# Kernel tuning notes

Hardware: AMD Instinct MI355X
Metric: run time of the kernel (lower is better)

The kernel has to match this reference:

```python
import jax, jax.numpy as jnp
import numpy as np
from jax import lax

MAX_OBJ = 100
IOU_THRES = 0.45
SCORE_THRES = 0.25
MAX_WH = 7680.0

# xywh -> xyxy conversion matrix (same as ONNX_ORT.convert_matrix)
CONVERT = jnp.array([[1, 0, 1, 0],
                     [0, 1, 0, 1],
                     [-0.5, 0, 0.5, 0],
                     [0, -0.5, 0, 0.5]], dtype=jnp.float32)


def _iou_one_vs_all(box, boxes):
    # box: [4] xyxy, boxes: [N,4] xyxy
    x1 = jnp.maximum(box[0], boxes[:, 0])
    y1 = jnp.maximum(box[1], boxes[:, 1])
    x2 = jnp.minimum(box[2], boxes[:, 2])
    y2 = jnp.minimum(box[3], boxes[:, 3])
    inter = jnp.clip(x2 - x1, 0.0) * jnp.clip(y2 - y1, 0.0)
    a = (box[2] - box[0]) * (box[3] - box[1])
    b = (boxes[:, 2] - boxes[:, 0]) * (boxes[:, 3] - boxes[:, 1])
    return inter / (a + b - inter + 1e-9)


def _nms_indices(nmsbox, max_score):
    # Greedy class-offset NMS; returns [MAX_OBJ] indices, -1 for padding.
    valid0 = max_score >= SCORE_THRES

    def step(valid, _):
        s = jnp.where(valid, max_score, -1.0)
        i = jnp.argmax(s)
        ok = s[i] >= SCORE_THRES
        iou = _iou_one_vs_all(nmsbox[i], nmsbox)
        valid = valid & (iou <= IOU_THRES)
        valid = valid.at[i].set(False)
        return valid, jnp.where(ok, i, -1)

    _, idxs = lax.scan(step, valid0, None, length=MAX_OBJ)
    return idxs


def _forward(x1, x2, num_labels1, num_labels2):
    B, N1, _ = x1.shape
    N2 = x2.shape[1]
    # pad x1 class scores with zeros for model2's labels (appended at end)
    x1p = jnp.concatenate([x1, jnp.zeros((B, N1, num_labels2), x1.dtype)], axis=2)
    # pad x2: insert zeros for model1's labels between conf and its own classes
    x2p = jnp.concatenate([x2[:, :, 0:5],
                           jnp.zeros((B, N2, num_labels1), x2.dtype),
                           x2[:, :, 5:]], axis=2)
    x = jnp.concatenate([x1p, x2p], axis=1)  # [B, N1+N2, 5+C1+C2]

    boxes = x[:, :, :4] @ CONVERT            # xywh -> xyxy, [B,N,4]
    conf = x[:, :, 4:5]
    scores = x[:, :, 5:] * conf              # [B,N,C]
    max_score = scores.max(axis=2)           # [B,N]
    cat_id = scores.argmax(axis=2)           # [B,N]
    # class-offset boxes so NMS is class-aware
    nmsbox = boxes + cat_id[..., None].astype(boxes.dtype) * MAX_WH

    idxs = jax.vmap(_nms_indices)(lax.stop_gradient(nmsbox),
                                  lax.stop_gradient(max_score))  # [B,MAX_OBJ]
    mask = idxs >= 0
    si = jnp.maximum(idxs, 0)
    sel_boxes = jnp.take_along_axis(boxes, si[..., None], axis=1)      # [B,MAX_OBJ,4]
    sel_cat = jnp.take_along_axis(cat_id, si, axis=1).astype(boxes.dtype)
    sel_score = jnp.take_along_axis(max_score, si, axis=1)

    mf = mask.astype(boxes.dtype)
    Xcol = jnp.where(mask, jnp.arange(B)[:, None], -1).astype(boxes.dtype)
    out = jnp.concatenate([Xcol[..., None],
                           sel_boxes * mf[..., None],
                           (sel_cat * mf)[..., None],
                           (sel_score * mf)[..., None]], axis=2)
    return out.reshape(B * MAX_OBJ, 7)


def setup_inputs() -> dict:
    key = jax.random.key(0)
    k1, k2 = jax.random.split(key)
    x1 = jax.random.uniform(k1, (4, 25200, 85), dtype=jnp.float32)
    x2 = jax.random.uniform(k2, (4, 25200, 25), dtype=jnp.float32)
    return {"x1": x1, "x2": x2, "num_labels1": 80, "num_labels2": 20}


def reference(x1, x2, num_labels1, num_labels2):
    return _forward(x1, x2, num_labels1, num_labels2)
```

## Files before the change

### kernel.cpp

```cpp
#include <hip/hip_runtime.h>
#include <stdint.h>

#pragma clang fp contract(off)

#define BATCH 4
#define N1 25200
#define NROW 50400
#define NCLS 100
#define TOT (BATCH*NROW)
#define CAPB 2048
#define SCORE_T 0.25f
#define IOU_T 0.45f
#define MAXWH 7680.0f

#define X1_SLAB 64
#define X1_SPB 394
#define X2_SLAB 256
#define X2_SPB 99

#define NKK 12600
#define NIT 49
#define NTAIL 56

typedef unsigned long long u64;

__device__ __forceinline__ u64 pack_key(unsigned sb, int n, int cid) {
    return ((u64)sb << 32) | ((u64)(unsigned)((n ^ 0xFFFF) & 0xFFFF) << 8) | (u64)(unsigned)cid;
}

__device__ __forceinline__ bool sup_test(float inter, float sum) {
    float d = (sum - inter) + 1e-9f;
    float t1 = IOU_T * d;
    bool hi = inter > t1 * 1.00001f;
    bool lo = inter < t1 * 0.99999f;
    if (__builtin_expect(!(hi || lo), 0)) return (inter / d) > IOU_T;
    return hi;
}

__device__ __forceinline__ float rl(float v, int srcLane) {
    return __int_as_float(__builtin_amdgcn_readlane(__float_as_int(v), srcLane));
}

__device__ __forceinline__ void blk2bucket(int blk, int& b, int& c) {
    if (blk < BATCH * 20) { b = blk / 20; c = 80 + (blk - b * 20); }
    else { int z = blk - BATCH * 20; b = z / 80; c = z - b * 80; }
}

__device__ __forceinline__ int prefix_ge(const u64* list, int cnt, u64 T) {
    int lo = 0, hi = cnt;
    while (lo < hi) {
        int mid = (lo + hi) >> 1;
        if (list[mid] >= T) lo = mid + 1; else hi = mid;
    }
    return lo;
}

__device__ __forceinline__ void sort_desc(u64* sk, int L, int t) {
    bool act = (t * 8) < L;
    u64 r[8];
    if (act) {
#pragma unroll
        for (int e = 0; e < 8; ++e) r[e] = sk[t * 8 + e];
    }
    for (int k = 2; k <= L; k <<= 1) {
        for (int j = k >> 1; j > 0; j >>= 1) {
            if (j >= 512) {
                if (act) {
#pragma unroll
                    for (int e = 0; e < 8; ++e) sk[t * 8 + e] = r[e];
                }
                __syncthreads();
                if (act) {
                    bool iAmLo = (t & (j >> 3)) == 0;
                    bool descSeg = (t & (k >> 3)) == 0;
                    bool takeMax = (descSeg == iAmLo);
#pragma unroll
                    for (int e = 0; e < 8; ++e) {
                        u64 u = r[e];
                        u64 v = sk[(t * 8 + e) ^ j];
                        bool uGE = (u >= v);
                        r[e] = (takeMax == uGE) ? u : v;
                    }
                }
                __syncthreads();
            } else if (j >= 8) {
                if (act) {
                    int dt = j >> 3;
                    bool iAmLo = (t & dt) == 0;
                    bool descSeg = (t & (k >> 3)) == 0;
                    bool takeMax = (descSeg == iAmLo);
#pragma unroll
                    for (int e = 0; e < 8; ++e) {
                        u64 u = r[e];
                        u64 v = __shfl_xor(u, dt, 64);
                        bool uGE = (u >= v);
                        r[e] = (takeMax == uGE) ? u : v;
                    }
                }
            } else {
                if (act) {
#pragma unroll
                    for (int e = 0; e < 8; ++e) {
                        if (!(e & j)) {
                            int e2 = e | j;
                            bool descSeg = (k >= 8) ? ((t & (k >> 3)) == 0)
                                                    : ((e & k) == 0);
                            u64 lo = r[e], hi = r[e2];
                            bool sw = descSeg ? (lo < hi) : (lo > hi);
                            if (sw) { r[e] = hi; r[e2] = lo; }
                        }
                    }
                }
            }
        }
    }
    if (act) {
#pragma unroll
        for (int e = 0; e < 8; ++e) sk[t * 8 + e] = r[e];
    }
    __syncthreads();
}

__global__ __launch_bounds__(256) void k_rows(const float* __restrict__ x1,
                                              const float* __restrict__ x2,
                                              float4* __restrict__ boxes4,
                                              u64* __restrict__ rowKey) {
    __shared__ float4 ld4[1600];
    float* ld = (float*)ld4;
    int blk = blockIdx.x;
    int t = threadIdx.x;
    const int NX1 = BATCH * X1_SPB;
    if (blk < NX1) {
        int b = blk / X1_SPB, s = blk - b * X1_SPB;
        int r0 = s * X1_SLAB;
        int nr = min(X1_SLAB, N1 - r0);
        const float4* src = (const float4*)(x1 + ((size_t)b * N1 + r0) * 85);
        int count4 = (nr * 85) >> 2;
        for (int i = t; i < count4; i += 256) ld4[i] = src[i];
        __syncthreads();
        int row = t >> 2, sub = t & 3;
        if (row < nr) {
            const float* p = ld + row * 85;
            float conf = p[4];
            u64 key = 0ULL;
            int base = sub * 20;
            for (int c = 0; c < 20; ++c) {
                int j = base + c;
                float v = p[5 + j] * conf;
                u64 kk = ((u64)__float_as_uint(v) << 32) | (unsigned)~(unsigned)j;
                if (kk > key) key = kk;
            }
            u64 o;
            o = __shfl_xor(key, 1, 64); if (o > key) key = o;
            o = __shfl_xor(key, 2, 64); if (o > key) key = o;
            if (sub == 0) {
                float best = __uint_as_float((unsigned)(key >> 32));
                int bestj = ~(unsigned)key;
                int n = r0 + row;
                int r = b * NROW + n;
                u64 outk = 0ULL;
                if (best >= SCORE_T) {
                    float cx = p[0], cy = p[1], w = p[2], h = p[3];
                    boxes4[r] = make_float4(cx - 0.5f * w, cy - 0.5f * h,
                                            cx + 0.5f * w, cy + 0.5f * h);
                    outk = pack_key((unsigned)(key >> 32), n, bestj);
                }
                rowKey[r] = outk;
            }
        }
    } else {
        int blk2 = blk - NX1;
        int b = blk2 / X2_SPB, s = blk2 - b * X2_SPB;
        int r0 = s * X2_SLAB;
        int nr = min(X2_SLAB, N1 - r0);
        const float4* src = (const float4*)(x2 + ((size_t)b * N1 + r0) * 25);
        int count4 = (nr * 25) >> 2;
        for (int i = t; i < count4; i += 256) ld4[i] = src[i];
        __syncthreads();
        if (t < nr) {
            const float* p = ld + t * 25;
            float conf = p[4];
            float best = 0.0f; int bestj = 0;
            for (int j2 = 0; j2 < 20; ++j2) {
                float v = p[5 + j2] * conf;
                if (v > best) { best = v; bestj = 80 + j2; }
            }
            int n = N1 + r0 + t;
            int r = b * NROW + n;
            u64 outk = 0ULL;
            if (best >= SCORE_T) {
                float cx = p[0], cy = p[1], w = p[2], h = p[3];
                boxes4[r] = make_float4(cx - 0.5f * w, cy - 0.5f * h,
                                        cx + 0.5f * w, cy + 0.5f * h);
                outk = pack_key(__float_as_uint(best), n, bestj);
            }
            rowKey[r] = outk;
        }
    }
}

__global__ __launch_bounds__(256) void k_nms(const float4* __restrict__ boxes4,
                                             const u64* __restrict__ rowKey,
                                             u64* __restrict__ accKey,
                                             int* __restrict__ accCnt) {
    __shared__ u64 sk[CAPB];
    __shared__ float4 cQ[CAPB];
    __shared__ float4 accQ[100];
    __shared__ float accA[100];
    __shared__ int wsum[4];
    int b, c; blk2bucket(blockIdx.x, b, c);
    int bucket = b * NCLS + c;
    int t = threadIdx.x;
    int lane = t & 63, wid = t >> 6;

    int rowBase = (c >= 80) ? N1 : 0;
    const ulonglong2* rk2 = (const ulonglong2*)(rowKey + (size_t)b * NROW + rowBase);

    int cnt = 0;
#pragma unroll 4
    for (int it = 0; it < NIT; ++it) {
        ulonglong2 kk = rk2[t + (it << 8)];
        cnt += ((kk.x != 0ULL) && ((int)(kk.x & 0xFF) == c)) ? 1 : 0;
        cnt += ((kk.y != 0ULL) && ((int)(kk.y & 0xFF) == c)) ? 1 : 0;
    }
    if (t < NTAIL) {
        ulonglong2 kk = rk2[NIT * 256 + t];
        cnt += ((kk.x != 0ULL) && ((int)(kk.x & 0xFF) == c)) ? 1 : 0;
        cnt += ((kk.y != 0ULL) && ((int)(kk.y & 0xFF) == c)) ? 1 : 0;
    }
    int inc = cnt;
    for (int o = 1; o < 64; o <<= 1) {
        int v = __shfl_up(inc, o, 64);
        if (lane >= o) inc += v;
    }
    if (lane == 63) wsum[wid] = inc;
    __syncthreads();
    int cnt0 = wsum[0] + wsum[1] + wsum[2] + wsum[3];
    if (cnt0 == 0) { if (t == 0) accCnt[bucket] = 0; return; }
    int woff = 0;
    for (int w = 0; w < wid; ++w) woff += wsum[w];
    int pos = woff + inc - cnt;
    cnt0 = min(cnt0, CAPB);
#pragma unroll 4
    for (int it = 0; it < NIT; ++it) {
        ulonglong2 kk = rk2[t + (it << 8)];
        if ((kk.x != 0ULL) && ((int)(kk.x & 0xFF) == c)) { if (pos < CAPB) sk[pos] = kk.x; ++pos; }
        if ((kk.y != 0ULL) && ((int)(kk.y & 0xFF) == c)) { if (pos < CAPB) sk[pos] = kk.y; ++pos; }
    }
    if (t < NTAIL) {
        ulonglong2 kk = rk2[NIT * 256 + t];
        if ((kk.x != 0ULL) && ((int)(kk.x & 0xFF) == c)) { if (pos < CAPB) sk[pos] = kk.x; ++pos; }
        if ((kk.y != 0ULL) && ((int)(kk.y & 0xFF) == c)) { if (pos < CAPB) sk[pos] = kk.y; ++pos; }
    }
    int L = 512; while (L < cnt0) L <<= 1;
    for (int i = cnt0 + t; i < L; i += 256) sk[i] = 0ULL;
    __syncthreads();
    sort_desc(sk, L, t);

    float off = (float)c * MAXWH;
    for (int i = t; i < cnt0; i += 256) {
        u64 k = sk[i];
        int n = 0xFFFF ^ (int)((k >> 8) & 0xFFFF);
        float4 v = boxes4[b * NROW + n];
        v.x += off; v.y += off; v.z += off; v.w += off;
        cQ[i] = v;
    }
    __syncthreads();
    if (t >= 64) return;

    int m = 0;
    for (int base = 0; base < cnt0 && m < 100; base += 64) {
        int j = base + lane;
        bool alive = (j < cnt0);
        float4 a = make_float4(0.f, 0.f, 0.f, 0.f);
        float aA = 0.f; u64 myKey = 0ULL;
        if (alive) {
            myKey = sk[j];
            a = cQ[j];
            aA = (a.z - a.x) * (a.w - a.y);
        }
        int k2 = 0;
        while (k2 < m) {
            if (__ballot(alive) == 0ULL) break;
            int rem = m - k2;
            if (rem >= 8) {
#pragma unroll
                for (int u = 0; u < 8; ++u) {
                    float4 q = accQ[k2 + u];
                    float qa = accA[k2 + u];
                    float xx1 = fmaxf(a.x, q.x), yy1 = fmaxf(a.y, q.y);
                    float xx2 = fminf(a.z, q.z), yy2 = fminf(a.w, q.w);
                    float inter = fmaxf(xx2 - xx1, 0.f) * fmaxf(yy2 - yy1, 0.f);
                    alive = alive && !sup_test(inter, qa + aA);
                }
                k2 += 8;
            } else {
                for (int u = 0; u < rem; ++u) {
                    float4 q = accQ[k2 + u];
                    float qa = accA[k2 + u];
                    float xx1 = fmaxf(a.x, q.x), yy1 = fmaxf(a.y, q.y);
                    float xx2 = fminf(a.z, q.z), yy2 = fminf(a.w, q.w);
                    float inter = fmaxf(xx2 - xx1, 0.f) * fmaxf(yy2 - yy1, 0.f);
                    alive = alive && !sup_test(inter, qa + aA);
                }
                k2 = m;
            }
        }
        u64 av = __ballot(alive);
        while (av != 0ULL && m < 100) {
            int f = __builtin_ctzll(av);
            float qx = rl(a.x, f), qy = rl(a.y, f);
            float qz = rl(a.z, f), qw = rl(a.w, f);
            float qa = rl(aA, f);
            if (lane == f) {
                accQ[m] = a; accA[m] = aA;
                accKey[(size_t)bucket * 100 + m] = myKey;
                alive = false;
            }
            ++m;
            if (alive) {
                float xx1 = fmaxf(a.x, qx), yy1 = fmaxf(a.y, qy);
                float xx2 = fminf(a.z, qz), yy2 = fminf(a.w, qw);
                float inter = fmaxf(xx2 - xx1, 0.f) * fmaxf(yy2 - yy1, 0.f);
                alive = !sup_test(inter, qa + aA);
            }
            av = __ballot(alive);
        }
    }
    if (lane == 0) accCnt[bucket] = m;
}

__global__ __launch_bounds__(256) void k_merge(const float4* __restrict__ boxes4,
                                               const u64* __restrict__ accKey,
                                               const int* __restrict__ accCnt,
                                               float* __restrict__ out) {
    __shared__ u64 sk[1024];
    __shared__ u64 head[NCLS];
    __shared__ int cnts[NCLS];
    __shared__ int pc[NCLS];
    int b = blockIdx.x, t = threadIdx.x;
    const u64* base = accKey + (size_t)b * NCLS * 100;
    if (t < NCLS) {
        int cc = accCnt[b * NCLS + t];
        cnts[t] = cc;
        head[t] = (cc > 0) ? base[t * 100] : 0ULL;
    }
    __syncthreads();
    int S = 0, ne = 0; u64 mn = ~0ULL;
    for (int c = 0; c < NCLS; ++c) {
        int cc = cnts[c];
        S += cc;
        if (cc > 0) { ++ne; u64 h = head[c]; if (h < mn) mn = h; }
    }
    u64 T;
    bool bisect;
    if (S <= 900)            { T = 0ULL; bisect = false; }
    else if (ne == NCLS)     { T = mn;   bisect = false; }
    else                     { T = 0ULL; bisect = true;  }
    if (t < NCLS) pc[t] = bisect ? 0 : prefix_ge(base + t * 100, cnts[t], T);
    __syncthreads();
    int G = 0;
    for (int c = 0; c < NCLS; ++c) G += pc[c];
    if (G > 1000) bisect = true;
    if (bisect) {
        u64 lo = 0ULL, hi = ~0ULL;
        for (int it = 0; it < 64; ++it) {
            u64 mid = lo + ((hi - lo) >> 1);
            if (t < NCLS) pc[t] = prefix_ge(base + t * 100, cnts[t], mid);
            __syncthreads();
            int cnt = 0;
            for (int c = 0; c < NCLS; ++c) cnt += pc[c];
            if (cnt >= 100 && cnt <= 1000) { T = mid; G = cnt; break; }
            if (cnt < 100) hi = mid; else lo = mid;
            __syncthreads();
        }
    }
    if (t < NCLS) {
        int off = 0;
        for (int c = 0; c < t; ++c) off += pc[c];
        int p = pc[t];
        for (int j = 0; j < p; ++j) sk[off + j] = base[t * 100 + j];
    }
    for (int i = G + t; i < 1024; i += 256) sk[i] = 0ULL;
    __syncthreads();
    sort_desc(sk, 1024, t);
    if (t < 100) {
        u64 k = sk[t];
        float* o7 = out + (size_t)(b * 100 + t) * 7;
        if (k == 0ULL) {
            o7[0] = -1.0f;
            o7[1] = 0.0f; o7[2] = 0.0f; o7[3] = 0.0f;
            o7[4] = 0.0f; o7[5] = 0.0f; o7[6] = 0.0f;
        } else {
            int n = 0xFFFF ^ (int)((k >> 8) & 0xFFFF);
            int cid = (int)(k & 0xFF);
            float4 bx = boxes4[b * NROW + n];
            o7[0] = (float)b;
            o7[1] = bx.x; o7[2] = bx.y; o7[3] = bx.z; o7[4] = bx.w;
            o7[5] = (float)cid;
            o7[6] = __uint_as_float((unsigned)(k >> 32));
        }
    }
}

extern "C" void kernel_launch(void* const* d_in, const int* in_sizes, int n_in,
                              void* d_out, int out_size, void* d_ws, size_t ws_size,
                              hipStream_t stream) {
    const float* x1 = (const float*)d_in[0];
    const float* x2 = (const float*)d_in[1];
    float* out = (float*)d_out;

    float4* boxes4 = (float4*)d_ws;
    u64* rowKey = (u64*)(boxes4 + TOT);
    u64* accKey = rowKey + TOT;
    int* accCnt = (int*)(accKey + (size_t)BATCH * NCLS * 100);

    int rowBlocks = BATCH * X1_SPB + BATCH * X2_SPB;
    k_rows<<<rowBlocks, 256, 0, stream>>>(x1, x2, boxes4, rowKey);
    k_nms<<<BATCH * NCLS, 256, 0, stream>>>(boxes4, rowKey, accKey, accCnt);
    k_merge<<<BATCH, 256, 0, stream>>>(boxes4, accKey, accCnt, out);
}
```

Baseline: 148.3 us.

## Bucket candidate keys per class with atomics instead of rescanning all rows

The row kernel now appends each passing candidate's key to a per-(batch,class) bucket using an atomic fill counter. This replaces the dense rowKey array that every NMS block had to scan twice (count, then compact). Each NMS block then reads only its own bucket, and the per-candidate shared-memory writes are deferred until after the greedy loop. This adds atomic contention, a memset launch and a lower per-class capacity (CAPB 1280). Bucket order is now nondeterministic, but the sort restores it. The selected box's area is also recomputed rather than read across lanes.

```diff
diff --git a/kernel.cpp b/kernel.cpp
--- a/kernel.cpp
+++ b/kernel.cpp
@@ -8,7 +8,7 @@
 #define NROW 50400
 #define NCLS 100
 #define TOT (BATCH*NROW)
-#define CAPB 2048
+#define CAPB 1280
 #define SCORE_T 0.25f
 #define IOU_T 0.45f
 #define MAXWH 7680.0f
@@ -17,10 +17,6 @@
 #define X1_SPB 394
 #define X2_SLAB 256
 #define X2_SPB 99
-
-#define NKK 12600
-#define NIT 49
-#define NTAIL 56
 
 typedef unsigned long long u64;
 
@@ -124,7 +120,8 @@
 __global__ __launch_bounds__(256) void k_rows(const float* __restrict__ x1,
                                               const float* __restrict__ x2,
                                               float4* __restrict__ boxes4,
-                                              u64* __restrict__ rowKey) {
+                                              u64* __restrict__ csrKey,
+                                              int* __restrict__ fill) {
     __shared__ float4 ld4[1600];
     float* ld = (float*)ld4;
     int blk = blockIdx.x;
@@ -156,16 +153,18 @@
             if (sub == 0) {
                 float best = __uint_as_float((unsigned)(key >> 32));
                 int bestj = ~(unsigned)key;
-                int n = r0 + row;
-                int r = b * NROW + n;
-                u64 outk = 0ULL;
                 if (best >= SCORE_T) {
+                    int n = r0 + row;
+                    int r = b * NROW + n;
                     float cx = p[0], cy = p[1], w = p[2], h = p[3];
                     boxes4[r] = make_float4(cx - 0.5f * w, cy - 0.5f * h,
                                             cx + 0.5f * w, cy + 0.5f * h);
-                    outk = pack_key((unsigned)(key >> 32), n, bestj);
-                }
-                rowKey[r] = outk;
+                    int bucket = b * NCLS + bestj;
+                    int pos = atomicAdd(&fill[bucket], 1);
+                    if (pos < CAPB)
+                        csrKey[(size_t)bucket * CAPB + pos] =
+                            pack_key((unsigned)(key >> 32), n, bestj);
+                }
             }
         }
     } else {
@@ -185,78 +184,42 @@
                 float v = p[5 + j2] * conf;
                 if (v > best) { best = v; bestj = 80 + j2; }
             }
-            int n = N1 + r0 + t;
-            int r = b * NROW + n;
-            u64 outk = 0ULL;
             if (best >= SCORE_T) {
+                int n = N1 + r0 + t;
+                int r = b * NROW + n;
                 float cx = p[0], cy = p[1], w = p[2], h = p[3];
                 boxes4[r] = make_float4(cx - 0.5f * w, cy - 0.5f * h,
                                         cx + 0.5f * w, cy + 0.5f * h);
-                outk = pack_key(__float_as_uint(best), n, bestj);
-            }
-            rowKey[r] = outk;
+                int bucket = b * NCLS + bestj;
+                int pos = atomicAdd(&fill[bucket], 1);
+                if (pos < CAPB)
+                    csrKey[(size_t)bucket * CAPB + pos] =
+                        pack_key(__float_as_uint(best), n, bestj);
+            }
         }
     }
 }
 
 __global__ __launch_bounds__(256) void k_nms(const float4* __restrict__ boxes4,
-                                             const u64* __restrict__ rowKey,
+                                             const u64* __restrict__ csrKey,
+                                             const int* __restrict__ fill,
                                              u64* __restrict__ accKey,
                                              int* __restrict__ accCnt) {
-    __shared__ u64 sk[CAPB];
+    __shared__ u64 sk[2048];
     __shared__ float4 cQ[CAPB];
     __shared__ float4 accQ[100];
     __shared__ float accA[100];
-    __shared__ int wsum[4];
     int b, c; blk2bucket(blockIdx.x, b, c);
     int bucket = b * NCLS + c;
     int t = threadIdx.x;
-    int lane = t & 63, wid = t >> 6;
-
-    int rowBase = (c >= 80) ? N1 : 0;
-    const ulonglong2* rk2 = (const ulonglong2*)(rowKey + (size_t)b * NROW + rowBase);
-
-    int cnt = 0;
-#pragma unroll 4
-    for (int it = 0; it < NIT; ++it) {
-        ulonglong2 kk = rk2[t + (it << 8)];
-        cnt += ((kk.x != 0ULL) && ((int)(kk.x & 0xFF) == c)) ? 1 : 0;
-        cnt += ((kk.y != 0ULL) && ((int)(kk.y & 0xFF) == c)) ? 1 : 0;
-    }
-    if (t < NTAIL) {
-        ulonglong2 kk = rk2[NIT * 256 + t];
-        cnt += ((kk.x != 0ULL) && ((int)(kk.x & 0xFF) == c)) ? 1 : 0;
-        cnt += ((kk.y != 0ULL) && ((int)(kk.y & 0xFF) == c)) ? 1 : 0;
-    }
-    int inc = cnt;
-    for (int o = 1; o < 64; o <<= 1) {
-        int v = __shfl_up(inc, o, 64);
-        if (lane >= o) inc += v;
-    }
-    if (lane == 63) wsum[wid] = inc;
-    __syncthreads();
-    int cnt0 = wsum[0] + wsum[1] + wsum[2] + wsum[3];
+    int lane = t & 63;
+    int cnt0 = min(fill[bucket], CAPB);
     if (cnt0 == 0) { if (t == 0) accCnt[bucket] = 0; return; }
-    int woff = 0;
-    for (int w = 0; w < wid; ++w) woff += wsum[w];
-    int pos = woff + inc - cnt;
-    cnt0 = min(cnt0, CAPB);
-#pragma unroll 4
-    for (int it = 0; it < NIT; ++it) {
-        ulonglong2 kk = rk2[t + (it << 8)];
-        if ((kk.x != 0ULL) && ((int)(kk.x & 0xFF) == c)) { if (pos < CAPB) sk[pos] = kk.x; ++pos; }
-        if ((kk.y != 0ULL) && ((int)(kk.y & 0xFF) == c)) { if (pos < CAPB) sk[pos] = kk.y; ++pos; }
-    }
-    if (t < NTAIL) {
-        ulonglong2 kk = rk2[NIT * 256 + t];
-        if ((kk.x != 0ULL) && ((int)(kk.x & 0xFF) == c)) { if (pos < CAPB) sk[pos] = kk.x; ++pos; }
-        if ((kk.y != 0ULL) && ((int)(kk.y & 0xFF) == c)) { if (pos < CAPB) sk[pos] = kk.y; ++pos; }
-    }
+    const u64* src = csrKey + (size_t)bucket * CAPB;
     int L = 512; while (L < cnt0) L <<= 1;
-    for (int i = cnt0 + t; i < L; i += 256) sk[i] = 0ULL;
+    for (int i = t; i < L; i += 256) sk[i] = (i < cnt0) ? src[i] : 0ULL;
     __syncthreads();
     sort_desc(sk, L, t);
-
     float off = (float)c * MAXWH;
     for (int i = t; i < cnt0; i += 256) {
         u64 k = sk[i];
@@ -307,24 +270,25 @@
             }
         }
         u64 av = __ballot(alive);
+        int accIdx = -1;
         while (av != 0ULL && m < 100) {
             int f = __builtin_ctzll(av);
             float qx = rl(a.x, f), qy = rl(a.y, f);
             float qz = rl(a.z, f), qw = rl(a.w, f);
-            float qa = rl(aA, f);
-            if (lane == f) {
-                accQ[m] = a; accA[m] = aA;
-                accKey[(size_t)bucket * 100 + m] = myKey;
-                alive = false;
-            }
+            if (lane == f) { accIdx = m; alive = false; }
             ++m;
             if (alive) {
+                float qa = (qz - qx) * (qw - qy);
                 float xx1 = fmaxf(a.x, qx), yy1 = fmaxf(a.y, qy);
                 float xx2 = fminf(a.z, qz), yy2 = fminf(a.w, qw);
                 float inter = fmaxf(xx2 - xx1, 0.f) * fmaxf(yy2 - yy1, 0.f);
                 alive = !sup_test(inter, qa + aA);
             }
             av = __ballot(alive);
+        }
+        if (accIdx >= 0) {
+            accQ[accIdx] = a; accA[accIdx] = aA;
+            accKey[(size_t)bucket * 100 + accIdx] = myKey;
         }
     }
     if (lane == 0) accCnt[bucket] = m;
@@ -411,12 +375,15 @@
     float* out = (float*)d_out;
 
     float4* boxes4 = (float4*)d_ws;
-    u64* rowKey = (u64*)(boxes4 + TOT);
-    u64* accKey = rowKey + TOT;
-    int* accCnt = (int*)(accKey + (size_t)BATCH * NCLS * 100);
+    u64* csrKey = (u64*)(boxes4 + TOT);
+    u64* accKey = csrKey + (size_t)BATCH * NCLS * CAPB;
+    int* fill   = (int*)(accKey + (size_t)BATCH * NCLS * 100);
+    int* accCnt = fill + BATCH * NCLS;
+
+    hipMemsetAsync(fill, 0, sizeof(int) * BATCH * NCLS, stream);
 
     int rowBlocks = BATCH * X1_SPB + BATCH * X2_SPB;
-    k_rows<<<rowBlocks, 256, 0, stream>>>(x1, x2, boxes4, rowKey);
-    k_nms<<<BATCH * NCLS, 256, 0, stream>>>(boxes4, rowKey, accKey, accCnt);
+    k_rows<<<rowBlocks, 256, 0, stream>>>(x1, x2, boxes4, csrKey, fill);
+    k_nms<<<BATCH * NCLS, 256, 0, stream>>>(boxes4, csrKey, fill, accKey, accCnt);
     k_merge<<<BATCH, 256, 0, stream>>>(boxes4, accKey, accCnt, out);
 }
```

New measurement: 203.0 us. +36.9%, slower.
